# Performance work log

Measured on AMD Instinct MI355X. Metric: run time of the kernel, lower is better.

Reference implementation:

```python
import jax, jax.numpy as jnp
import numpy as np

L, D, H, d = 16, 1024, 16, 64
NB, BS = 1024, 16        # num physical blocks, block size (tokens per block)
START_POS = 16368        # T = START_POS + L = 16384
SCALE = 1.0 / np.sqrt(d)


def setup_inputs() -> dict:
    key = jax.random.key(0)
    ks = jax.random.split(key, 5)
    return {
        "x": jax.random.normal(ks[0], (L, D), jnp.float32),
        "k_pool": jax.random.normal(ks[1], (NB, BS, H, d), jnp.float32),
        "v_pool": jax.random.normal(ks[2], (NB, BS, H, d), jnp.float32),
        "W_attn": jax.random.normal(ks[3], (D, 3 * D), jnp.float32) * 0.02,
        "b_attn": jnp.zeros((3 * D,), jnp.float32),
        "W_proj": jax.random.normal(ks[4], (D, D), jnp.float32) * 0.02,
        "b_proj": jnp.zeros((D,), jnp.float32),
        "block_ids": jnp.arange(NB, dtype=jnp.int64),
        "start_pos": START_POS,
    }


def reference(x, k_pool, v_pool, W_attn, b_attn, W_proj, b_proj, block_ids, start_pos):
    # QKV projection
    qkv = x @ W_attn + b_attn                      # [L, 3D]
    q, k, v = jnp.split(qkv, 3, axis=-1)
    q = q.reshape(L, H, d)
    k = k.reshape(L, H, d)
    v = v.reshape(L, H, d)

    # paged write of new K/V into the pool
    pos = start_pos + jnp.arange(L)                # logical positions of new tokens
    blk = block_ids[pos // BS]                     # physical block per token
    off = pos % BS
    k_pool = k_pool.at[blk, off].set(k)
    v_pool = v_pool.at[blk, off].set(v)

    # paged read of the full prefix [0, T)
    T = start_pos + L
    k_pos = jnp.arange(T)
    kb = block_ids[k_pos // BS]
    ko = k_pos % BS
    k_cache = k_pool[kb, ko]                       # [T, H, d]
    v_cache = v_pool[kb, ko]                       # [T, H, d]

    # attention: scores [H, L, T]
    scores = jnp.einsum("lhd,thd->hlt", q, k_cache) * SCALE
    mask = k_pos[None, :] > pos[:, None]           # [L, T] future positions
    scores = jnp.where(mask[None, :, :], -jnp.inf, scores)
    attn = jax.nn.softmax(scores.astype(jnp.float32), axis=-1).astype(scores.dtype)

    out = jnp.einsum("hlt,thd->lhd", attn, v_cache).reshape(L, D)
    return out @ W_proj + b_proj
```

## Files before the change

kernel.cpp:

```cpp
#include <hip/hip_runtime.h>
#include <math.h>

#define L_TOK 16
#define DMODEL 1024
#define NHEAD 16
#define DHEAD 64
#define NBLK 1024
#define BSZ 16
#define START_POS_C 16368
#define TTOT 16384
#define SPLITS 128
#define CHUNK 128
#define KSPLIT 16
#define QSCALE (0.125f * 1.4426950408889634f)

#define OFF_QKVP 0
#define OFF_QW   (OFF_QKVP + KSPLIT * L_TOK * 3 * DMODEL)
#define OFF_ACC  (OFF_QW + NHEAD * L_TOK * DHEAD)
#define OFF_M    (OFF_ACC + NHEAD * SPLITS * L_TOK * DHEAD)
#define OFF_SE   (OFF_M + NHEAD * SPLITS * L_TOK)
#define OFF_ATTN (OFF_SE + NHEAD * SPLITS * L_TOK)
#define OFF_PROJP (OFF_ATTN + L_TOK * DMODEL)

template<int R>
__device__ __forceinline__ float dppror(float x) {
    if constexpr (R == 0) {
        return x;
    } else {
        int i = __builtin_amdgcn_update_dpp(0, __float_as_int(x), 0x120 + R, 0xF, 0xF, false);
        return __int_as_float(i);
    }
}
template<int R>
__device__ __forceinline__ int dppror_i(int x) {
    if constexpr (R == 0) return x;
    else return __builtin_amdgcn_update_dpp(0, x, 0x120 + R, 0xF, 0xF, false);
}

template<int R>
__device__ __forceinline__ float qk_step(const float* ql, const float* kk) {
    float d0 = 0.f, d1 = 0.f, d2 = 0.f, d3 = 0.f;
#pragma unroll
    for (int c = 0; c < 4; ++c) {
        d0 = fmaf(ql[c],      dppror<R>(kk[c]),      d0);
        d1 = fmaf(ql[4 + c],  dppror<R>(kk[4 + c]),  d1);
        d2 = fmaf(ql[8 + c],  dppror<R>(kk[8 + c]),  d2);
        d3 = fmaf(ql[12 + c], dppror<R>(kk[12 + c]), d3);
    }
    return (d0 + d1) + (d2 + d3);
}

template<int R>
__device__ __forceinline__ void pv_step(float p, const float* vv, float* acc) {
#pragma unroll
    for (int c = 0; c < 16; ++c)
        acc[c] = fmaf(p, dppror<R>(vv[c]), acc[c]);
}

__global__ __launch_bounds__(256) void gemm_part(const float* __restrict__ x,
                                                 const float* __restrict__ W,
                                                 float* __restrict__ part,
                                                 int ncols) {
    const int lane = threadIdx.x & 63;
    const int wv = threadIdx.x >> 6;
    const int n = blockIdx.x * 64 + lane;
    const int k0 = blockIdx.y * (DMODEL / KSPLIT);
    const float* xr = x + (size_t)(wv * 4) * DMODEL;
    float a0 = 0.f, a1 = 0.f, a2 = 0.f, a3 = 0.f;
#pragma unroll 8
    for (int k = k0; k < k0 + DMODEL / KSPLIT; ++k) {
        float w = W[(size_t)k * ncols + n];
        a0 = fmaf(xr[k], w, a0);
        a1 = fmaf(xr[DMODEL + k], w, a1);
        a2 = fmaf(xr[2 * DMODEL + k], w, a2);
        a3 = fmaf(xr[3 * DMODEL + k], w, a3);
    }
    size_t base = ((size_t)blockIdx.y * L_TOK + wv * 4) * ncols + n;
    part[base] = a0;
    part[base + (size_t)ncols] = a1;
    part[base + 2 * (size_t)ncols] = a2;
    part[base + 3 * (size_t)ncols] = a3;
}

__global__ __launch_bounds__(256) void qkv_reduce_scatter(const float* __restrict__ part,
                                                          const float* __restrict__ b_attn,
                                                          const int* __restrict__ block_ids,
                                                          float* __restrict__ qws,
                                                          float* __restrict__ kpool,
                                                          float* __restrict__ vpool) {
    int tid = blockIdx.x * 256 + threadIdx.x;
    int n = tid % (3 * DMODEL);
    int l = tid / (3 * DMODEL);
    float s = b_attn[n];
#pragma unroll
    for (int kb = 0; kb < KSPLIT; ++kb)
        s += part[((size_t)kb * L_TOK + l) * (3 * DMODEL) + n];
    int sec = n >> 10;
    int m = n & (DMODEL - 1);
    int h = m >> 6;
    int dd = m & 63;
    if (sec == 0) {
        qws[(h * L_TOK + l) * DHEAD + dd] = s * QSCALE;
    } else {
        int pos = START_POS_C + l;
        int blk = block_ids[pos >> 4];
        int off = pos & 15;
        size_t idx = (((size_t)blk * BSZ + off) * NHEAD + h) * DHEAD + dd;
        if (sec == 1) kpool[idx] = s;
        else          vpool[idx] = s;
    }
}

__global__ __launch_bounds__(64) void paged_attn(const float* __restrict__ kpool,
                                                 const float* __restrict__ vpool,
                                                 const int* __restrict__ block_ids,
                                                 const float* __restrict__ qws,
                                                 float* __restrict__ accws,
                                                 float* __restrict__ m_arr,
                                                 float* __restrict__ se_arr) {
    const int h = blockIdx.x;
    const int s = blockIdx.y;
    const int lane = threadIdx.x;
    const int t = lane & 15;
    const int g = lane >> 4;

    int pbs[CHUNK / 16];
#pragma unroll
    for (int i = 0; i < CHUNK / 16; ++i)
        pbs[i] = block_ids[s * (CHUNK / 16) + i];

    float ql[16];
    {
        const float4* qp = (const float4*)(qws + ((size_t)(h * L_TOK + t)) * DHEAD + g * 16);
#pragma unroll
        for (int c = 0; c < 4; ++c) {
            float4 v = qp[c];
            ql[c * 4 + 0] = v.x; ql[c * 4 + 1] = v.y;
            ql[c * 4 + 2] = v.z; ql[c * 4 + 3] = v.w;
        }
    }

    float acc[16];
#pragma unroll
    for (int c = 0; c < 16; ++c) acc[c] = 0.f;
    float m_run = -INFINITY, se_run = 0.f;

    for (int tile = 0; tile < CHUNK / 16; ++tile) {
        const int tbase = s * CHUNK + tile * 16;
        const int pb = pbs[tile];
        const size_t rowbase = (((size_t)pb * BSZ + t) * NHEAD + h) * DHEAD + g * 16;

        float kk[16], vv[16];
        {
            const float4* k4 = (const float4*)(kpool + rowbase);
            const float4* v4 = (const float4*)(vpool + rowbase);
#pragma unroll
            for (int c = 0; c < 4; ++c) {
                float4 a = k4[c];
                kk[c * 4 + 0] = a.x; kk[c * 4 + 1] = a.y;
                kk[c * 4 + 2] = a.z; kk[c * 4 + 3] = a.w;
            }
#pragma unroll
            for (int c = 0; c < 4; ++c) {
                float a = 0.f; (void)a;
                float4 b = v4[c];
                vv[c * 4 + 0] = b.x; vv[c * 4 + 1] = b.y;
                vv[c * 4 + 2] = b.z; vv[c * 4 + 3] = b.w;
            }
        }

        float s16[16];
        s16[0]  = qk_step<0>(ql, kk);   s16[1]  = qk_step<1>(ql, kk);
        s16[2]  = qk_step<2>(ql, kk);   s16[3]  = qk_step<3>(ql, kk);
        s16[4]  = qk_step<4>(ql, kk);   s16[5]  = qk_step<5>(ql, kk);
        s16[6]  = qk_step<6>(ql, kk);   s16[7]  = qk_step<7>(ql, kk);
        s16[8]  = qk_step<8>(ql, kk);   s16[9]  = qk_step<9>(ql, kk);
        s16[10] = qk_step<10>(ql, kk);  s16[11] = qk_step<11>(ql, kk);
        s16[12] = qk_step<12>(ql, kk);  s16[13] = qk_step<13>(ql, kk);
        s16[14] = qk_step<14>(ql, kk);  s16[15] = qk_step<15>(ql, kk);

#pragma unroll
        for (int r = 0; r < 16; ++r) {
            s16[r] += __shfl_xor(s16[r], 16, 64);
            s16[r] += __shfl_xor(s16[r], 32, 64);
        }

        if (tbase + 15 > START_POS_C) {
            const int tv = t;
#define MASKJ(R) { int j = dppror_i<R>(tv); if (tbase + j > START_POS_C + t) s16[R] = -INFINITY; }
            MASKJ(0)  MASKJ(1)  MASKJ(2)  MASKJ(3)
            MASKJ(4)  MASKJ(5)  MASKJ(6)  MASKJ(7)
            MASKJ(8)  MASKJ(9)  MASKJ(10) MASKJ(11)
            MASKJ(12) MASKJ(13) MASKJ(14) MASKJ(15)
#undef MASKJ
        }

        float m16 = s16[0];
#pragma unroll
        for (int r = 1; r < 16; ++r) m16 = fmaxf(m16, s16[r]);
        const float m_new = fmaxf(m_run, m16);
        const float alpha = exp2f(m_run - m_new);
        float p[16];
        float tsum = 0.f;
#pragma unroll
        for (int r = 0; r < 16; ++r) {
            p[r] = exp2f(s16[r] - m_new);
            tsum += p[r];
        }
        se_run = se_run * alpha + tsum;
        m_run = m_new;
#pragma unroll
        for (int c = 0; c < 16; ++c) acc[c] *= alpha;

        pv_step<0>(p[0], vv, acc);    pv_step<1>(p[1], vv, acc);
        pv_step<2>(p[2], vv, acc);    pv_step<3>(p[3], vv, acc);
        pv_step<4>(p[4], vv, acc);    pv_step<5>(p[5], vv, acc);
        pv_step<6>(p[6], vv, acc);    pv_step<7>(p[7], vv, acc);
        pv_step<8>(p[8], vv, acc);    pv_step<9>(p[9], vv, acc);
        pv_step<10>(p[10], vv, acc);  pv_step<11>(p[11], vv, acc);
        pv_step<12>(p[12], vv, acc);  pv_step<13>(p[13], vv, acc);
        pv_step<14>(p[14], vv, acc);  pv_step<15>(p[15], vv, acc);
    }

    const size_t obase = (((size_t)(h * SPLITS + s)) * L_TOK + t) * DHEAD + g * 16;
    float4* op = (float4*)(accws + obase);
    op[0] = make_float4(acc[0],  acc[1],  acc[2],  acc[3]);
    op[1] = make_float4(acc[4],  acc[5],  acc[6],  acc[7]);
    op[2] = make_float4(acc[8],  acc[9],  acc[10], acc[11]);
    op[3] = make_float4(acc[12], acc[13], acc[14], acc[15]);
    if (g == 0) {
        const size_t mb = (size_t)(h * SPLITS + s) * L_TOK + t;
        m_arr[mb] = m_run;
        se_arr[mb] = se_run;
    }
}

__global__ __launch_bounds__(256) void combine(const float* __restrict__ accws,
                                               const float* __restrict__ m_arr,
                                               const float* __restrict__ se_arr,
                                               float* __restrict__ attnws) {
    const int h = blockIdx.x >> 4;
    const int l = blockIdx.x & 15;
    const int w = threadIdx.x >> 6;
    const int lane = threadIdx.x & 63;
    __shared__ float sm[4], sse[4], sacc[4][64];

    float M = -INFINITY, num = 0.f, den = 0.f;
#pragma unroll 4
    for (int s = w; s < SPLITS; s += 4) {
        const size_t idx = (size_t)(h * SPLITS + s) * L_TOK + l;
        const float ms = m_arr[idx];
        const float ses = se_arr[idx];
        const float a = accws[idx * DHEAD + lane];
        const float Mn = fmaxf(M, ms);
        const float c_old = exp2f(M - Mn);
        const float c_new = exp2f(ms - Mn);
        num = num * c_old + a * c_new;
        den = den * c_old + ses * c_new;
        M = Mn;
    }
    if (lane == 0) { sm[w] = M; sse[w] = den; }
    sacc[w][lane] = num;
    __syncthreads();
    if (w == 0) {
        const float M0 = fmaxf(fmaxf(sm[0], sm[1]), fmaxf(sm[2], sm[3]));
        float nn = 0.f, dd = 0.f;
#pragma unroll
        for (int i = 0; i < 4; ++i) {
            const float wgt = exp2f(sm[i] - M0);
            nn = fmaf(wgt, sacc[i][lane], nn);
            dd = fmaf(wgt, sse[i], dd);
        }
        attnws[(size_t)l * DMODEL + h * DHEAD + lane] = nn / dd;
    }
}

__global__ __launch_bounds__(256) void proj_reduce(const float* __restrict__ part,
                                                   const float* __restrict__ bias,
                                                   float* __restrict__ out) {
    int tid = blockIdx.x * 256 + threadIdx.x;
    int n = tid & (DMODEL - 1);
    int l = tid >> 10;
    float s = bias[n];
#pragma unroll
    for (int kb = 0; kb < KSPLIT; ++kb)
        s += part[((size_t)kb * L_TOK + l) * DMODEL + n];
    out[tid] = s;
}

extern "C" void kernel_launch(void* const* d_in, const int* in_sizes, int n_in,
                              void* d_out, int out_size, void* d_ws, size_t ws_size,
                              hipStream_t stream) {
    const float* x       = (const float*)d_in[0];
    float* kpool         = (float*)d_in[1];
    float* vpool         = (float*)d_in[2];
    const float* W_attn  = (const float*)d_in[3];
    const float* b_attn  = (const float*)d_in[4];
    const float* W_proj  = (const float*)d_in[5];
    const float* b_proj  = (const float*)d_in[6];
    const int* block_ids = (const int*)d_in[7];
    float* ws  = (float*)d_ws;
    float* out = (float*)d_out;

    gemm_part<<<dim3(48, KSPLIT), 256, 0, stream>>>(x, W_attn, ws + OFF_QKVP, 3 * DMODEL);
    qkv_reduce_scatter<<<192, 256, 0, stream>>>(ws + OFF_QKVP, b_attn, block_ids,
                                                ws + OFF_QW, kpool, vpool);
    paged_attn<<<dim3(NHEAD, SPLITS), 64, 0, stream>>>(kpool, vpool, block_ids,
                                                       ws + OFF_QW, ws + OFF_ACC,
                                                       ws + OFF_M, ws + OFF_SE);
    combine<<<NHEAD * L_TOK, 256, 0, stream>>>(ws + OFF_ACC, ws + OFF_M, ws + OFF_SE,
                                               ws + OFF_ATTN);
    gemm_part<<<dim3(16, KSPLIT), 256, 0, stream>>>(ws + OFF_ATTN, W_proj, ws + OFF_PROJP, DMODEL);
    proj_reduce<<<64, 256, 0, stream>>>(ws + OFF_PROJP, b_proj, out);
}
```

Baseline: 231.6 us.

## Compute paged attention QK and PV with fp16 MFMA instead of DPP FMAs

Rewrites the split-K paged attention kernel so Q·K and P·V run on fp16 matrix-core MFMA instructions instead of scalar FMAs with DPP lane rotations. K and Q are converted to fp16 in registers, V is transposed through a double-buffered LDS tile, and two 16-token blocks are processed per iteration. The aim is to cut VALU work in the attention stage. In exchange it lowers precision to fp16 for the inputs and probabilities, adds LDS traffic, and writes the outputs in a strided layout.

```diff
diff --git a/kernel.cpp b/kernel.cpp
--- a/kernel.cpp
+++ b/kernel.cpp
@@ -22,40 +22,13 @@
 #define OFF_ATTN (OFF_SE + NHEAD * SPLITS * L_TOK)
 #define OFF_PROJP (OFF_ATTN + L_TOK * DMODEL)
 
-template<int R>
-__device__ __forceinline__ float dppror(float x) {
-    if constexpr (R == 0) {
-        return x;
-    } else {
-        int i = __builtin_amdgcn_update_dpp(0, __float_as_int(x), 0x120 + R, 0xF, 0xF, false);
-        return __int_as_float(i);
-    }
-}
-template<int R>
-__device__ __forceinline__ int dppror_i(int x) {
-    if constexpr (R == 0) return x;
-    else return __builtin_amdgcn_update_dpp(0, x, 0x120 + R, 0xF, 0xF, false);
-}
-
-template<int R>
-__device__ __forceinline__ float qk_step(const float* ql, const float* kk) {
-    float d0 = 0.f, d1 = 0.f, d2 = 0.f, d3 = 0.f;
-#pragma unroll
-    for (int c = 0; c < 4; ++c) {
-        d0 = fmaf(ql[c],      dppror<R>(kk[c]),      d0);
-        d1 = fmaf(ql[4 + c],  dppror<R>(kk[4 + c]),  d1);
-        d2 = fmaf(ql[8 + c],  dppror<R>(kk[8 + c]),  d2);
-        d3 = fmaf(ql[12 + c], dppror<R>(kk[12 + c]), d3);
-    }
-    return (d0 + d1) + (d2 + d3);
-}
-
-template<int R>
-__device__ __forceinline__ void pv_step(float p, const float* vv, float* acc) {
-#pragma unroll
-    for (int c = 0; c < 16; ++c)
-        acc[c] = fmaf(p, dppror<R>(vv[c]), acc[c]);
-}
+typedef _Float16 half2_t __attribute__((ext_vector_type(2)));
+typedef _Float16 half4_t __attribute__((ext_vector_type(4)));
+typedef _Float16 half8_t __attribute__((ext_vector_type(8)));
+typedef float float4v __attribute__((ext_vector_type(4)));
+
+union H8 { _Float16 h[8]; half8_t v; };
+union H4 { _Float16 h[4]; half4_t v; };
 
 __global__ __launch_bounds__(256) void gemm_part(const float* __restrict__ x,
                                                  const float* __restrict__ W,
@@ -121,115 +94,146 @@
     const int h = blockIdx.x;
     const int s = blockIdx.y;
     const int lane = threadIdx.x;
-    const int t = lane & 15;
-    const int g = lane >> 4;
-
-    int pbs[CHUNK / 16];
-#pragma unroll
-    for (int i = 0; i < CHUNK / 16; ++i)
-        pbs[i] = block_ids[s * (CHUNK / 16) + i];
-
-    float ql[16];
+    const int c = lane & 15;
+    const int quad = lane >> 4;
+
+    __shared__ float VT[2][64][36];
+
+    H8 qb0, qb1;
     {
-        const float4* qp = (const float4*)(qws + ((size_t)(h * L_TOK + t)) * DHEAD + g * 16);
-#pragma unroll
-        for (int c = 0; c < 4; ++c) {
-            float4 v = qp[c];
-            ql[c * 4 + 0] = v.x; ql[c * 4 + 1] = v.y;
-            ql[c * 4 + 2] = v.z; ql[c * 4 + 3] = v.w;
+        const float* qr = qws + ((size_t)(h * L_TOK + c)) * DHEAD + quad * 8;
+        float4 q0 = *(const float4*)(qr);
+        float4 q1 = *(const float4*)(qr + 4);
+        float4 q2 = *(const float4*)(qr + 32);
+        float4 q3 = *(const float4*)(qr + 36);
+        qb0.h[0] = (_Float16)q0.x; qb0.h[1] = (_Float16)q0.y;
+        qb0.h[2] = (_Float16)q0.z; qb0.h[3] = (_Float16)q0.w;
+        qb0.h[4] = (_Float16)q1.x; qb0.h[5] = (_Float16)q1.y;
+        qb0.h[6] = (_Float16)q1.z; qb0.h[7] = (_Float16)q1.w;
+        qb1.h[0] = (_Float16)q2.x; qb1.h[1] = (_Float16)q2.y;
+        qb1.h[2] = (_Float16)q2.z; qb1.h[3] = (_Float16)q2.w;
+        qb1.h[4] = (_Float16)q3.x; qb1.h[5] = (_Float16)q3.y;
+        qb1.h[6] = (_Float16)q3.z; qb1.h[7] = (_Float16)q3.w;
+    }
+
+    float4v acc[4];
+#pragma unroll
+    for (int i = 0; i < 4; ++i) acc[i] = (float4v){0.f, 0.f, 0.f, 0.f};
+    float m_run = -INFINITY, se_run = 0.f;
+
+    const int blk0 = s * (CHUNK / 16);
+
+#pragma unroll 2
+    for (int grp = 0; grp < CHUNK / 32; ++grp) {
+        const int tb = s * CHUNK + grp * 32;
+        const int buf = grp & 1;
+        const int pb0 = block_ids[blk0 + 2 * grp];
+        const int pb1 = block_ids[blk0 + 2 * grp + 1];
+
+        const float* kr0 = kpool + (((size_t)pb0 * BSZ + c) * NHEAD + h) * DHEAD + quad * 8;
+        const float* kr1 = kpool + (((size_t)pb1 * BSZ + c) * NHEAD + h) * DHEAD + quad * 8;
+        const float* vr0 = vpool + (((size_t)pb0 * BSZ + c) * NHEAD + h) * DHEAD + quad * 8;
+        const float* vr1 = vpool + (((size_t)pb1 * BSZ + c) * NHEAD + h) * DHEAD + quad * 8;
+        float4 k0a = *(const float4*)(kr0);      float4 k0b = *(const float4*)(kr0 + 4);
+        float4 k0c = *(const float4*)(kr0 + 32); float4 k0d = *(const float4*)(kr0 + 36);
+        float4 k1a = *(const float4*)(kr1);      float4 k1b = *(const float4*)(kr1 + 4);
+        float4 k1c = *(const float4*)(kr1 + 32); float4 k1d = *(const float4*)(kr1 + 36);
+        float4 v0a = *(const float4*)(vr0);      float4 v0b = *(const float4*)(vr0 + 4);
+        float4 v0c = *(const float4*)(vr0 + 32); float4 v0d = *(const float4*)(vr0 + 36);
+        float4 v1a = *(const float4*)(vr1);      float4 v1b = *(const float4*)(vr1 + 4);
+        float4 v1c = *(const float4*)(vr1 + 32); float4 v1d = *(const float4*)(vr1 + 36);
+
+        {
+            float* w0 = &VT[buf][quad * 8][c];
+            w0[0*36]=v0a.x; w0[1*36]=v0a.y; w0[2*36]=v0a.z; w0[3*36]=v0a.w;
+            w0[4*36]=v0b.x; w0[5*36]=v0b.y; w0[6*36]=v0b.z; w0[7*36]=v0b.w;
+            float* w1 = &VT[buf][32 + quad * 8][c];
+            w1[0*36]=v0c.x; w1[1*36]=v0c.y; w1[2*36]=v0c.z; w1[3*36]=v0c.w;
+            w1[4*36]=v0d.x; w1[5*36]=v0d.y; w1[6*36]=v0d.z; w1[7*36]=v0d.w;
+            float* w2 = &VT[buf][quad * 8][16 + c];
+            w2[0*36]=v1a.x; w2[1*36]=v1a.y; w2[2*36]=v1a.z; w2[3*36]=v1a.w;
+            w2[4*36]=v1b.x; w2[5*36]=v1b.y; w2[6*36]=v1b.z; w2[7*36]=v1b.w;
+            float* w3 = &VT[buf][32 + quad * 8][16 + c];
+            w3[0*36]=v1c.x; w3[1*36]=v1c.y; w3[2*36]=v1c.z; w3[3*36]=v1c.w;
+            w3[4*36]=v1d.x; w3[5*36]=v1d.y; w3[6*36]=v1d.z; w3[7*36]=v1d.w;
         }
-    }
-
-    float acc[16];
-#pragma unroll
-    for (int c = 0; c < 16; ++c) acc[c] = 0.f;
-    float m_run = -INFINITY, se_run = 0.f;
-
-    for (int tile = 0; tile < CHUNK / 16; ++tile) {
-        const int tbase = s * CHUNK + tile * 16;
-        const int pb = pbs[tile];
-        const size_t rowbase = (((size_t)pb * BSZ + t) * NHEAD + h) * DHEAD + g * 16;
-
-        float kk[16], vv[16];
-        {
-            const float4* k4 = (const float4*)(kpool + rowbase);
-            const float4* v4 = (const float4*)(vpool + rowbase);
-#pragma unroll
-            for (int c = 0; c < 4; ++c) {
-                float4 a = k4[c];
-                kk[c * 4 + 0] = a.x; kk[c * 4 + 1] = a.y;
-                kk[c * 4 + 2] = a.z; kk[c * 4 + 3] = a.w;
-            }
-#pragma unroll
-            for (int c = 0; c < 4; ++c) {
-                float a = 0.f; (void)a;
-                float4 b = v4[c];
-                vv[c * 4 + 0] = b.x; vv[c * 4 + 1] = b.y;
-                vv[c * 4 + 2] = b.z; vv[c * 4 + 3] = b.w;
+
+        const float4v z4 = {0.f, 0.f, 0.f, 0.f};
+        H8 ka, kb;
+        ka.h[0]=(_Float16)k0a.x; ka.h[1]=(_Float16)k0a.y; ka.h[2]=(_Float16)k0a.z; ka.h[3]=(_Float16)k0a.w;
+        ka.h[4]=(_Float16)k0b.x; ka.h[5]=(_Float16)k0b.y; ka.h[6]=(_Float16)k0b.z; ka.h[7]=(_Float16)k0b.w;
+        kb.h[0]=(_Float16)k0c.x; kb.h[1]=(_Float16)k0c.y; kb.h[2]=(_Float16)k0c.z; kb.h[3]=(_Float16)k0c.w;
+        kb.h[4]=(_Float16)k0d.x; kb.h[5]=(_Float16)k0d.y; kb.h[6]=(_Float16)k0d.z; kb.h[7]=(_Float16)k0d.w;
+        float4v st0 = __builtin_amdgcn_mfma_f32_16x16x32_f16(ka.v, qb0.v, z4, 0, 0, 0);
+        st0 = __builtin_amdgcn_mfma_f32_16x16x32_f16(kb.v, qb1.v, st0, 0, 0, 0);
+        ka.h[0]=(_Float16)k1a.x; ka.h[1]=(_Float16)k1a.y; ka.h[2]=(_Float16)k1a.z; ka.h[3]=(_Float16)k1a.w;
+        ka.h[4]=(_Float16)k1b.x; ka.h[5]=(_Float16)k1b.y; ka.h[6]=(_Float16)k1b.z; ka.h[7]=(_Float16)k1b.w;
+        kb.h[0]=(_Float16)k1c.x; kb.h[1]=(_Float16)k1c.y; kb.h[2]=(_Float16)k1c.z; kb.h[3]=(_Float16)k1c.w;
+        kb.h[4]=(_Float16)k1d.x; kb.h[5]=(_Float16)k1d.y; kb.h[6]=(_Float16)k1d.z; kb.h[7]=(_Float16)k1d.w;
+        float4v st1 = __builtin_amdgcn_mfma_f32_16x16x32_f16(ka.v, qb0.v, z4, 0, 0, 0);
+        st1 = __builtin_amdgcn_mfma_f32_16x16x32_f16(kb.v, qb1.v, st1, 0, 0, 0);
+
+        if (tb + 31 > START_POS_C) {
+#pragma unroll
+            for (int r = 0; r < 4; ++r) {
+                if (tb + 4 * quad + r > START_POS_C + c)      st0[r] = -INFINITY;
+                if (tb + 16 + 4 * quad + r > START_POS_C + c) st1[r] = -INFINITY;
             }
         }
 
-        float s16[16];
-        s16[0]  = qk_step<0>(ql, kk);   s16[1]  = qk_step<1>(ql, kk);
-        s16[2]  = qk_step<2>(ql, kk);   s16[3]  = qk_step<3>(ql, kk);
-        s16[4]  = qk_step<4>(ql, kk);   s16[5]  = qk_step<5>(ql, kk);
-        s16[6]  = qk_step<6>(ql, kk);   s16[7]  = qk_step<7>(ql, kk);
-        s16[8]  = qk_step<8>(ql, kk);   s16[9]  = qk_step<9>(ql, kk);
-        s16[10] = qk_step<10>(ql, kk);  s16[11] = qk_step<11>(ql, kk);
-        s16[12] = qk_step<12>(ql, kk);  s16[13] = qk_step<13>(ql, kk);
-        s16[14] = qk_step<14>(ql, kk);  s16[15] = qk_step<15>(ql, kk);
-
-#pragma unroll
-        for (int r = 0; r < 16; ++r) {
-            s16[r] += __shfl_xor(s16[r], 16, 64);
-            s16[r] += __shfl_xor(s16[r], 32, 64);
+        float tm = fmaxf(fmaxf(fmaxf(st0[0], st0[1]), fmaxf(st0[2], st0[3])),
+                         fmaxf(fmaxf(st1[0], st1[1]), fmaxf(st1[2], st1[3])));
+        tm = fmaxf(tm, __shfl_xor(tm, 16, 64));
+        tm = fmaxf(tm, __shfl_xor(tm, 32, 64));
+        const float m_new = fmaxf(m_run, tm);
+        const float alpha = exp2f(m_run - m_new);
+        float p[8];
+        p[0] = exp2f(st0[0] - m_new); p[1] = exp2f(st0[1] - m_new);
+        p[2] = exp2f(st0[2] - m_new); p[3] = exp2f(st0[3] - m_new);
+        p[4] = exp2f(st1[0] - m_new); p[5] = exp2f(st1[1] - m_new);
+        p[6] = exp2f(st1[2] - m_new); p[7] = exp2f(st1[3] - m_new);
+        H4 pa0, pa1;
+        pa0.h[0]=(_Float16)p[0]; pa0.h[1]=(_Float16)p[1];
+        pa0.h[2]=(_Float16)p[2]; pa0.h[3]=(_Float16)p[3];
+        pa1.h[0]=(_Float16)p[4]; pa1.h[1]=(_Float16)p[5];
+        pa1.h[2]=(_Float16)p[6]; pa1.h[3]=(_Float16)p[7];
+        float ts = ((float)pa0.h[0] + (float)pa0.h[1]) + ((float)pa0.h[2] + (float)pa0.h[3])
+                 + ((float)pa1.h[0] + (float)pa1.h[1]) + ((float)pa1.h[2] + (float)pa1.h[3]);
+        ts += __shfl_xor(ts, 16, 64);
+        ts += __shfl_xor(ts, 32, 64);
+        se_run = se_run * alpha + ts;
+        m_run = m_new;
+
+        float ar[4];
+#pragma unroll
+        for (int r = 0; r < 4; ++r) ar[r] = __shfl(alpha, quad * 4 + r, 64);
+#pragma unroll
+        for (int ndv = 0; ndv < 4; ++ndv)
+#pragma unroll
+            for (int r = 0; r < 4; ++r) acc[ndv][r] *= ar[r];
+
+#pragma unroll
+        for (int tau = 0; tau < 2; ++tau) {
+            const half4_t pf = tau ? pa1.v : pa0.v;
+#pragma unroll
+            for (int ndv = 0; ndv < 4; ++ndv) {
+                float4 vb = *(const float4*)&VT[buf][16 * ndv + c][16 * tau + 4 * quad];
+                H4 bf;
+                bf.h[0] = (_Float16)vb.x; bf.h[1] = (_Float16)vb.y;
+                bf.h[2] = (_Float16)vb.z; bf.h[3] = (_Float16)vb.w;
+                acc[ndv] = __builtin_amdgcn_mfma_f32_16x16x16f16(pf, bf.v, acc[ndv], 0, 0, 0);
+            }
         }
-
-        if (tbase + 15 > START_POS_C) {
-            const int tv = t;
-#define MASKJ(R) { int j = dppror_i<R>(tv); if (tbase + j > START_POS_C + t) s16[R] = -INFINITY; }
-            MASKJ(0)  MASKJ(1)  MASKJ(2)  MASKJ(3)
-            MASKJ(4)  MASKJ(5)  MASKJ(6)  MASKJ(7)
-            MASKJ(8)  MASKJ(9)  MASKJ(10) MASKJ(11)
-            MASKJ(12) MASKJ(13) MASKJ(14) MASKJ(15)
-#undef MASKJ
-        }
-
-        float m16 = s16[0];
-#pragma unroll
-        for (int r = 1; r < 16; ++r) m16 = fmaxf(m16, s16[r]);
-        const float m_new = fmaxf(m_run, m16);
-        const float alpha = exp2f(m_run - m_new);
-        float p[16];
-        float tsum = 0.f;
-#pragma unroll
-        for (int r = 0; r < 16; ++r) {
-            p[r] = exp2f(s16[r] - m_new);
-            tsum += p[r];
-        }
-        se_run = se_run * alpha + tsum;
-        m_run = m_new;
-#pragma unroll
-        for (int c = 0; c < 16; ++c) acc[c] *= alpha;
-
-        pv_step<0>(p[0], vv, acc);    pv_step<1>(p[1], vv, acc);
-        pv_step<2>(p[2], vv, acc);    pv_step<3>(p[3], vv, acc);
-        pv_step<4>(p[4], vv, acc);    pv_step<5>(p[5], vv, acc);
-        pv_step<6>(p[6], vv, acc);    pv_step<7>(p[7], vv, acc);
-        pv_step<8>(p[8], vv, acc);    pv_step<9>(p[9], vv, acc);
-        pv_step<10>(p[10], vv, acc);  pv_step<11>(p[11], vv, acc);
-        pv_step<12>(p[12], vv, acc);  pv_step<13>(p[13], vv, acc);
-        pv_step<14>(p[14], vv, acc);  pv_step<15>(p[15], vv, acc);
-    }
-
-    const size_t obase = (((size_t)(h * SPLITS + s)) * L_TOK + t) * DHEAD + g * 16;
-    float4* op = (float4*)(accws + obase);
-    op[0] = make_float4(acc[0],  acc[1],  acc[2],  acc[3]);
-    op[1] = make_float4(acc[4],  acc[5],  acc[6],  acc[7]);
-    op[2] = make_float4(acc[8],  acc[9],  acc[10], acc[11]);
-    op[3] = make_float4(acc[12], acc[13], acc[14], acc[15]);
-    if (g == 0) {
-        const size_t mb = (size_t)(h * SPLITS + s) * L_TOK + t;
+    }
+
+    const size_t ob = (size_t)(h * SPLITS + s) * L_TOK * DHEAD;
+#pragma unroll
+    for (int ndv = 0; ndv < 4; ++ndv)
+#pragma unroll
+        for (int r = 0; r < 4; ++r)
+            accws[ob + (size_t)(4 * quad + r) * DHEAD + 16 * ndv + c] = acc[ndv][r];
+    if (quad == 0) {
+        const size_t mb = (size_t)(h * SPLITS + s) * L_TOK + c;
         m_arr[mb] = m_run;
         se_arr[mb] = se_run;
     }
```

New measurement: 207.8 us. -10.3%, faster.
